# Performance work log

Measured on AMD Instinct MI355X. Metric: run time of the kernel, lower is better.

Reference implementation:

```python
import jax, jax.numpy as jnp
import numpy as np

SHIFT, REDUCE = 1, 2
B, L, E, H = 128, 64, 512, 512
T = 2 * L - 1  # valid binary-parse transition sequence length


def _make_transitions(rng):
    # Random *valid* shift-reduce sequences: L shifts, L-1 reduces, stack ends at 1.
    trans = np.zeros((B, T), dtype=np.int32)
    for b in range(B):
        stack, buf = 0, L
        for t in range(T):
            ops_left = T - t
            can_shift = buf > 0 and stack < ops_left
            can_reduce = stack >= 2
            if can_shift and can_reduce:
                act = SHIFT if rng.random() < 0.5 else REDUCE
            elif can_shift:
                act = SHIFT
            else:
                act = REDUCE
            if act == SHIFT:
                buf -= 1; stack += 1
            else:
                stack -= 1
            trans[b, t] = act
    return trans


def setup_inputs() -> dict:
    key = jax.random.key(0)
    k1, k2, k3, k4 = jax.random.split(key, 4)
    sentence = jax.random.normal(k1, (B, L, E), dtype=jnp.float32)
    transitions = jnp.asarray(_make_transitions(np.random.default_rng(0)))
    W_word = jax.random.normal(k2, (E, 2 * H), dtype=jnp.float32) / np.sqrt(E).astype(np.float32)
    b_word = jnp.zeros((2 * H,), dtype=jnp.float32)
    W_left = jax.random.normal(k3, (H, 5 * H), dtype=jnp.float32) / np.sqrt(H).astype(np.float32)
    W_right = jax.random.normal(k4, (H, 5 * H), dtype=jnp.float32) / np.sqrt(H).astype(np.float32)
    b_reduce = jnp.zeros((5 * H,), dtype=jnp.float32)
    return {"sentence": sentence, "transitions": transitions, "W_word": W_word,
            "b_word": b_word, "W_left": W_left, "W_right": W_right, "b_reduce": b_reduce}


def reference(sentence, transitions, W_word, b_word, W_left, W_right, b_reduce):
    Bx, Lx, _ = sentence.shape
    Hx = W_left.shape[0]
    Tx = transitions.shape[1]
    # word projection (no_batch_norm=True, dropout=0 in this config)
    out = sentence @ W_word + b_word                      # [B, L, 2H]
    h_buf, c_buf = jnp.split(out, 2, axis=2)              # buffers, popped front-to-back
    rows = jnp.arange(Bx)
    ops_left_seq = jnp.arange(Tx, 0, -1, dtype=jnp.int32)
    init = (jnp.zeros((Bx, Lx, Hx), out.dtype),           # stack h
            jnp.zeros((Bx, Lx, Hx), out.dtype),           # stack c
            jnp.zeros((Bx,), jnp.int32),                  # stack ptr
            jnp.zeros((Bx,), jnp.int32))                  # buffer ptr

    def step(carry, xs):
        sh, sc, sp, bp = carry
        act, ops = xs
        act = jnp.where(sp > ops, REDUCE, act)            # forced reduce (discrete stack)
        is_red = act == REDUCE
        is_shf = act == SHIFT
        r_idx = jnp.clip(sp - 1, 0, Lx - 1)
        l_idx = jnp.clip(sp - 2, 0, Lx - 1)
        hl, cl = sh[rows, l_idx], sc[rows, l_idx]
        hr, cr = sh[rows, r_idx], sc[rows, r_idx]
        # TreeLSTM Reduce cell
        gates = hl @ W_left + hr @ W_right + b_reduce     # [B, 5H]
        g, i, f1, f2, o = jnp.split(gates, 5, axis=1)
        c_red = jnp.tanh(g) * jax.nn.sigmoid(i) + jax.nn.sigmoid(f1) * cl + jax.nn.sigmoid(f2) * cr
        h_red = jax.nn.sigmoid(o) * jnp.tanh(c_red)
        b_idx = jnp.clip(bp, 0, Lx - 1)
        h_shf, c_shf = h_buf[rows, b_idx], c_buf[rows, b_idx]
        w_idx = jnp.where(is_red, l_idx, jnp.clip(sp, 0, Lx - 1))
        h_cur, c_cur = sh[rows, w_idx], sc[rows, w_idx]
        m_red, m_shf = is_red[:, None], is_shf[:, None]
        wh = jnp.where(m_red, h_red, jnp.where(m_shf, h_shf, h_cur))
        wc = jnp.where(m_red, c_red, jnp.where(m_shf, c_shf, c_cur))
        sh = sh.at[rows, w_idx].set(wh)
        sc = sc.at[rows, w_idx].set(wc)
        sp = sp + is_shf.astype(jnp.int32) - is_red.astype(jnp.int32)
        bp = bp + is_shf.astype(jnp.int32)
        return (sh, sc, sp, bp), None

    (sh, sc, sp, bp), _ = jax.lax.scan(step, init, (transitions.T, ops_left_seq))
    return sh[rows, jnp.clip(sp - 1, 0, Lx - 1)]          # [B, H] top of each stack
```

## Files before the change

### kernel.cpp

```cpp
#include <hip/hip_runtime.h>
#include <hip/hip_bf16.h>


#define Bn 128
#define Ln 64
#define En 512
#define Hn 512
#define Tn 127
#define LEAF_ROWS (Bn*Ln)
#define NODE_ROWS (Bn*(Ln-1))
#define TOT_ROWS (LEAF_ROWS+NODE_ROWS)
#define NLVL 64
#define NXCD 8
#define CAPX 512
#define NBLK 512
#define FPAD 16
#define MAXRANK 96
#define SPIN_CAP (1<<22)
#define GATE_STRIDE (512*1024)
#define WLDS_BYTES 65536
#define PART_BYTES (4*2*16*20*4)
#define DYN_BYTES (WLDS_BYTES + PART_BYTES)

#define OFF_CENSUS 0
#define OFF_RANK   (OFF_CENSUS + NXCD*FPAD)
#define OFF_SFLAG  (OFF_RANK + NBLK*FPAD)
#define OFF_SGEN   (OFF_SFLAG + NBLK*FPAD)
#define OFF_FX     (OFF_SGEN + FPAD)
#define OFF_GX     (OFF_FX + NXCD*MAXRANK*FPAD)
#define BAR_INTS   (OFF_GX + NXCD*FPAD)

typedef __attribute__((ext_vector_type(8))) short bf16x8;
typedef __attribute__((ext_vector_type(4))) float f32x4;

static __device__ __forceinline__ float bf2f(unsigned short u){
  unsigned v = ((unsigned)u) << 16;
  float f; __builtin_memcpy(&f, &v, 4); return f;
}
static __device__ __forceinline__ unsigned short f2bf(float f){
  unsigned u; __builtin_memcpy(&u, &f, 4);
  u = u + 0x7FFFu + ((u >> 16) & 1u);
  return (unsigned short)(u >> 16);
}
static __device__ __forceinline__ float sigm(float x){
  return 1.0f / (1.0f + __expf(-x));
}
static __device__ __forceinline__ float tanh_fast(float x){
  x = fminf(fmaxf(x, -15.0f), 15.0f);
  float t = __expf(2.0f * x);
  return (t - 1.0f) / (t + 1.0f);
}
static __device__ __forceinline__ int xcc_id(){
  unsigned v;
  asm volatile("s_getreg_b32 %0, hwreg(HW_REG_XCC_ID)" : "=s"(v));
  return (int)(v & 7);
}

static __device__ __forceinline__ void xcd_barrier(int* bar, int x, int rank, int nx, int epoch){
  __syncthreads();
  int* fx = bar + OFF_FX + x * MAXRANK * FPAD;
  int* gx = bar + OFF_GX + x * FPAD;
  int nxl = min(nx, MAXRANK);
  if (rank == 0){
    for (int i = threadIdx.x + 1; i < nxl; i += 256){
      int c = 0;
      while (__hip_atomic_load(&fx[i * FPAD], __ATOMIC_RELAXED, __HIP_MEMORY_SCOPE_AGENT) < epoch && c < SPIN_CAP){
        __builtin_amdgcn_s_sleep(1); ++c;
      }
    }
    __syncthreads();
    if (threadIdx.x == 0)
      __hip_atomic_store(gx, epoch, __ATOMIC_RELAXED, __HIP_MEMORY_SCOPE_AGENT);
  } else {
    if (threadIdx.x == 0){
      __hip_atomic_store(&fx[rank * FPAD], epoch, __ATOMIC_RELAXED, __HIP_MEMORY_SCOPE_AGENT);
      int c = 0;
      while (__hip_atomic_load(gx, __ATOMIC_RELAXED, __HIP_MEMORY_SCOPE_AGENT) < epoch && c < SPIN_CAP){
        __builtin_amdgcn_s_sleep(2); ++c;
      }
    }
    __syncthreads();
  }
  asm volatile("" ::: "memory");
}


__global__ void cvt_vec4(const float4* __restrict__ x, ushort4* __restrict__ y, int n4){
  int i = blockIdx.x * 256 + threadIdx.x;
  if (i < n4){
    float4 v = x[i];
    ushort4 o;
    o.x = f2bf(v.x); o.y = f2bf(v.y); o.z = f2bf(v.z); o.w = f2bf(v.w);
    y[i] = o;
  }
}

__global__ void transpose_cvt(const float* __restrict__ src, unsigned short* __restrict__ dstT,
                              int CS, int DS, int koff){
  __shared__ float tile[32][33];
  int c0 = blockIdx.x * 32, r0 = blockIdx.y * 32;
  int tx = threadIdx.x, ty = threadIdx.y;
  for (int i = ty; i < 32; i += 8) tile[i][tx] = src[(size_t)(r0 + i) * CS + c0 + tx];
  __syncthreads();
  for (int i = ty; i < 32; i += 8)
    dstT[(size_t)(c0 + i) * DS + koff + r0 + tx] = f2bf(tile[tx][i]);
}

__global__ void precompute_ctrl(const int* __restrict__ trans,
                                int* __restrict__ srcL, int* __restrict__ srcR,
                                int* __restrict__ dstv, int* __restrict__ cnt,
                                int* __restrict__ outsrc, int* __restrict__ bar){
  __shared__ int stk[Bn][Ln + 1];
  __shared__ int scnt[NXCD * NLVL];
  __shared__ int smaxl[NXCD];
  int b = threadIdx.x;
  for (int i = b; i < NXCD * NLVL; i += 128) scnt[i] = 0;
  if (b < NXCD) smaxl[b] = 0;
  for (int i = b; i < BAR_INTS; i += 128) bar[i] = 0;
  __syncthreads();
  int x = b & 7;
  int sp = 0, bp = 0, nodecnt = 0;
  int act_next = trans[b * Tn];
  for (int t = 0; t < Tn; t++){
    int act = act_next;
    if (t + 1 < Tn) act_next = trans[b * Tn + t + 1];
    int ops = Tn - t;
    if (sp > ops) act = 2;
    if (act == 2){
      int R = stk[b][sp - 1], L = stk[b][sp - 2];
      int lvl = max(R >> 20, L >> 20) + 1;
      int slot = atomicAdd(&scnt[x * NLVL + lvl], 1);
      int base = (x * NLVL + lvl) * CAPX + slot;
      srcL[base] = (L & 0xFFFFF) * Hn;
      srcR[base] = (R & 0xFFFFF) * Hn;
      int noderow = LEAF_ROWS + b * (Ln - 1) + nodecnt;
      dstv[base] = noderow * Hn;
      stk[b][sp - 2] = noderow | (lvl << 20);
      sp -= 1; nodecnt++;
    } else {
      stk[b][sp] = b * Ln + min(bp, Ln - 1);
      sp += 1; bp += 1;
    }
  }
  int root = stk[b][max(sp - 1, 0)];
  outsrc[b] = (root & 0xFFFFF) * Hn;
  atomicMax(&smaxl[x], root >> 20);
  __syncthreads();
  for (int i = b; i < NXCD * NLVL; i += 128) cnt[i] = scnt[i];
  if (b < NXCD) cnt[NXCD * NLVL + b] = smaxl[b];
}

__global__ __launch_bounds__(256) void word_gemm(
    const unsigned short* __restrict__ SB, const unsigned short* __restrict__ WwT,
    const float* __restrict__ b_word,
    unsigned short* __restrict__ HB, float* __restrict__ CF){
  int mt = blockIdx.x;
  int nt = blockIdx.y;
  int tid = threadIdx.x, w = tid >> 6, lane = tid & 63;
  int wm = w >> 1, wn = w & 1;
  int rc = lane & 15, lg = lane >> 4;
  const unsigned short* ap0 = SB + (size_t)(mt * 64 + wm * 32 + rc) * En + lg * 8;
  const unsigned short* ap1 = ap0 + (size_t)16 * En;
  const unsigned short* bp0 = WwT + (size_t)(nt * 128 + wn * 64 + rc) * En + lg * 8;
  f32x4 acc[2][4];
  #pragma unroll
  for (int h = 0; h < 2; h++)
    #pragma unroll
    for (int nb = 0; nb < 4; nb++) acc[h][nb] = (f32x4){0.f,0.f,0.f,0.f};

  bf16x8 a0c = *(const bf16x8*)ap0;
  bf16x8 a1c = *(const bf16x8*)ap1;
  bf16x8 bc[4];
  #pragma unroll
  for (int nb = 0; nb < 4; nb++) bc[nb] = *(const bf16x8*)(bp0 + (size_t)nb * 16 * En);

  #pragma unroll
  for (int j = 0; j < 16; ++j){
    bf16x8 a0n, a1n, bn[4];
    if (j < 15){
      int kn = (j + 1) * 32;
      a0n = *(const bf16x8*)(ap0 + kn);
      a1n = *(const bf16x8*)(ap1 + kn);
      #pragma unroll
      for (int nb = 0; nb < 4; nb++)
        bn[nb] = *(const bf16x8*)(bp0 + (size_t)nb * 16 * En + kn);
    }
    #pragma unroll
    for (int nb = 0; nb < 4; nb++){
      acc[0][nb] = __builtin_amdgcn_mfma_f32_16x16x32_bf16(a0c, bc[nb], acc[0][nb], 0, 0, 0);
      acc[1][nb] = __builtin_amdgcn_mfma_f32_16x16x32_bf16(a1c, bc[nb], acc[1][nb], 0, 0, 0);
    }
    a0c = a0n; a1c = a1n;
    #pragma unroll
    for (int nb = 0; nb < 4; nb++) bc[nb] = bn[nb];
  }
  #pragma unroll
  for (int nb = 0; nb < 4; nb++){
    int col = nt * 128 + wn * 64 + nb * 16 + rc;
    float bw = b_word[col];
    #pragma unroll
    for (int h = 0; h < 2; h++){
      #pragma unroll
      for (int q = 0; q < 4; q++){
        int row = mt * 64 + wm * 32 + h * 16 + lg * 4 + q;
        float v = acc[h][nb][q] + bw;
        if (col < Hn) HB[(size_t)row * Hn + col] = f2bf(v);
        else          CF[(size_t)row * Hn + (col - Hn)] = v;
      }
    }
  }
}

template<bool LDSB>
static __device__ __forceinline__ void tile64(
    int u0, int t, int nr, const int* __restrict__ sL, const int* __restrict__ sR,
    const int* __restrict__ dl,
    unsigned short* __restrict__ HB, float* __restrict__ CF,
    const unsigned short* __restrict__ WT, const float* __restrict__ b_red,
    const unsigned short* __restrict__ wlds, int rc, int lg)
{
  int base = t * 64;
  int offL[4], offR[4];
  #pragma unroll
  for (int m = 0; m < 4; m++){
    int i = min(base + m * 16 + rc, nr - 1);
    offL[m] = sL[i]; offR[m] = sR[i];
  }
  f32x4 acc[5][4];
  #pragma unroll
  for (int g = 0; g < 5; g++)
    #pragma unroll
    for (int m = 0; m < 4; m++) acc[g][m] = (f32x4){0.f,0.f,0.f,0.f};

  int bswz = (rc & 7) << 3;
  const unsigned short* gb = WT + (size_t)(u0 + rc) * 1024 + lg * 8;

  bf16x8 a_cur[4], b_cur[3];
  #pragma unroll
  for (int m = 0; m < 4; m++) a_cur[m] = *(const bf16x8*)(HB + offL[m] + lg * 8);
  #pragma unroll
  for (int g = 0; g < 3; g++)
    b_cur[g] = *(const bf16x8*)(gb + (size_t)(g + 2) * GATE_STRIDE);

  #pragma unroll 4
  for (int j = 0; j < 32; ++j){
    bf16x8 a_nxt[4], b_nxt[3];
    if (j < 31){
      int kn = (j + 1) * 32 + lg * 8;
      #pragma unroll
      for (int m = 0; m < 4; m++){
        const unsigned short* ap = (j + 1 < 16) ? (HB + offL[m] + kn) : (HB + offR[m] + (kn - 512));
        a_nxt[m] = *(const bf16x8*)ap;
      }
      #pragma unroll
      for (int g = 0; g < 3; g++)
        b_nxt[g] = *(const bf16x8*)(gb + (size_t)(g + 2) * GATE_STRIDE + (j + 1) * 32);
    }
    int k = j * 32 + lg * 8;
    #pragma unroll
    for (int g = 0; g < 2; g++){
      bf16x8 bb;
      if (LDSB) bb = *(const bf16x8*)&wlds[(size_t)(g * 16 + rc) * 1024 + (k ^ bswz)];
      else      bb = *(const bf16x8*)(gb + (size_t)g * GATE_STRIDE + j * 32);
      #pragma unroll
      for (int m = 0; m < 4; m++)
        acc[g][m] = __builtin_amdgcn_mfma_f32_16x16x32_bf16(a_cur[m], bb, acc[g][m], 0, 0, 0);
    }
    #pragma unroll
    for (int g = 0; g < 3; g++){
      #pragma unroll
      for (int m = 0; m < 4; m++)
        acc[g + 2][m] = __builtin_amdgcn_mfma_f32_16x16x32_bf16(a_cur[m], b_cur[g], acc[g + 2][m], 0, 0, 0);
    }
    #pragma unroll
    for (int m = 0; m < 4; m++) a_cur[m] = a_nxt[m];
    #pragma unroll
    for (int g = 0; g < 3; g++) b_cur[g] = b_nxt[g];
  }
  int colu = u0 + rc;
  float bs[5];
  #pragma unroll
  for (int g = 0; g < 5; g++) bs[g] = b_red[g * Hn + colu];
  #pragma unroll
  for (int m = 0; m < 4; m++){
    #pragma unroll
    for (int q = 0; q < 4; q++){
      int i = base + m * 16 + lg * 4 + q;
      if (i < nr){
        int oL = sL[i], oR = sR[i], oD = dl[i];
        float gv = tanh_fast(acc[0][m][q] + bs[0]);
        float iv = sigm(acc[1][m][q] + bs[1]);
        float f1 = sigm(acc[2][m][q] + bs[2]);
        float f2 = sigm(acc[3][m][q] + bs[3]);
        float ov = sigm(acc[4][m][q] + bs[4]);
        float cl = __builtin_nontemporal_load(CF + oL + colu);
        float cr = __builtin_nontemporal_load(CF + oR + colu);
        float cv = gv * iv + f1 * cl + f2 * cr;
        float hv = ov * tanh_fast(cv);
        __builtin_nontemporal_store(cv, CF + oD + colu);
        HB[oD + colu] = f2bf(hv);
      }
    }
  }
}

static __device__ __forceinline__ void tile16(
    int u0, int t, int nr, const int* __restrict__ sL, const int* __restrict__ sR,
    const int* __restrict__ dl,
    unsigned short* __restrict__ HB, float* __restrict__ CF,
    const unsigned short* __restrict__ WT, const float* __restrict__ b_red,
    const unsigned short* __restrict__ wlds, float (*part)[2][16][20],
    int tid, int w, int rc, int lg)
{
  int base = t * 16;
  int er = tid >> 4, eu = tid & 15;
  int i0 = min(base + rc, nr - 1);
  int offA = (w >= 2) ? sR[i0] : sL[i0];
  int ie = min(base + er, nr - 1);
  int oL = sL[ie], oR = sR[ie], oD = dl[ie];
  int colu = u0 + eu;
  float cl = __builtin_nontemporal_load(CF + oL + colu);
  float cr = __builtin_nontemporal_load(CF + oR + colu);

  int k0 = w * 256;
  int abase = (w >= 2) ? (k0 - 512) : k0;
  const unsigned short* ap = HB + offA + abase + lg * 8;
  int bswz = (rc & 7) << 3;
  const unsigned short* gb = WT + (size_t)(u0 + rc) * 1024;

  f32x4 acc[5];
  #pragma unroll
  for (int g = 0; g < 5; g++) acc[g] = (f32x4){0.f,0.f,0.f,0.f};

  bf16x8 a_cur = *(const bf16x8*)ap;
  bf16x8 b_cur[3];
  #pragma unroll
  for (int g = 0; g < 3; g++)
    b_cur[g] = *(const bf16x8*)(gb + (size_t)(g + 2) * GATE_STRIDE + k0 + lg * 8);

  #pragma unroll
  for (int j = 0; j < 8; ++j){
    bf16x8 a_nxt, b_nxt[3];
    if (j < 7){
      a_nxt = *(const bf16x8*)(ap + (j + 1) * 32);
      #pragma unroll
      for (int g = 0; g < 3; g++)
        b_nxt[g] = *(const bf16x8*)(gb + (size_t)(g + 2) * GATE_STRIDE + k0 + (j + 1) * 32 + lg * 8);
    }
    int k = k0 + j * 32 + lg * 8;
    #pragma unroll
    for (int g = 0; g < 2; g++){
      bf16x8 bb = *(const bf16x8*)&wlds[(size_t)(g * 16 + rc) * 1024 + (k ^ bswz)];
      acc[g] = __builtin_amdgcn_mfma_f32_16x16x32_bf16(a_cur, bb, acc[g], 0, 0, 0);
    }
    #pragma unroll
    for (int g = 0; g < 3; g++)
      acc[g + 2] = __builtin_amdgcn_mfma_f32_16x16x32_bf16(a_cur, b_cur[g], acc[g + 2], 0, 0, 0);
    a_cur = a_nxt;
    #pragma unroll
    for (int g = 0; g < 3; g++) b_cur[g] = b_nxt[g];
  }
  float sg[5];
  #pragma unroll
  for (int r = 0; r < 3; ++r){
    int ng = (r < 2) ? 2 : 1;
    #pragma unroll
    for (int gi = 0; gi < 2; ++gi){
      if (gi < ng){
        int g = r * 2 + gi;
        #pragma unroll
        for (int q = 0; q < 4; q++) part[w][gi][lg * 4 + q][rc] = acc[g][q];
      }
    }
    __syncthreads();
    #pragma unroll
    for (int gi = 0; gi < 2; ++gi){
      if (gi < ng)
        sg[r * 2 + gi] = part[0][gi][er][eu] + part[1][gi][er][eu]
                       + part[2][gi][er][eu] + part[3][gi][er][eu];
    }
    __syncthreads();
  }
  int i = base + er;
  if (i < nr){
    float gv = tanh_fast(sg[0] + b_red[colu]);
    float iv = sigm(sg[1] + b_red[Hn + colu]);
    float f1 = sigm(sg[2] + b_red[2 * Hn + colu]);
    float f2 = sigm(sg[3] + b_red[3 * Hn + colu]);
    float ov = sigm(sg[4] + b_red[4 * Hn + colu]);
    float cv = gv * iv + f1 * cl + f2 * cr;
    float hv = ov * tanh_fast(cv);
    __builtin_nontemporal_store(cv, CF + oD + colu);
    HB[oD + colu] = f2bf(hv);
  }
  __syncthreads();
}

extern __shared__ char dynbuf[];

__global__ __launch_bounds__(256, 2) void tree_kernel(
    unsigned short* __restrict__ HB, float* __restrict__ CF,
    const unsigned short* __restrict__ WT, const float* __restrict__ b_red,
    const int* __restrict__ srcL, const int* __restrict__ srcR,
    const int* __restrict__ dstv, const int* __restrict__ cnt,
    const int* __restrict__ outsrc, float* __restrict__ out, int* bar){
  unsigned short* wlds = (unsigned short*)dynbuf;
  float (*part)[2][16][20] = (float(*)[2][16][20])(dynbuf + WLDS_BYTES);
  int bid = blockIdx.x;
  int tid = threadIdx.x, w = tid >> 6, lane = tid & 63;
  int rc = lane & 15, lg = lane >> 4;

  int x = xcc_id();
  if (tid == 0){
    int r = __hip_atomic_fetch_add(&bar[OFF_CENSUS + x * FPAD], 1,
                                   __ATOMIC_RELAXED, __HIP_MEMORY_SCOPE_AGENT);
    __hip_atomic_store(&bar[OFF_RANK + bid * FPAD], r, __ATOMIC_RELAXED, __HIP_MEMORY_SCOPE_AGENT);
  }
  __syncthreads();
  int rank = min(__hip_atomic_load(&bar[OFF_RANK + bid * FPAD], __ATOMIC_RELAXED, __HIP_MEMORY_SCOPE_AGENT),
                 MAXRANK - 1);
  int ub = rank & 31;
  int u0 = ub * 16;

  for (int gg = tid; gg < 4096; gg += 256){
    int row = gg >> 7;
    int k = (gg & 127) * 8;
    int u = row & 15, g = row >> 4;
    bf16x8 v = *(const bf16x8*)(WT + (size_t)(g * 512 + u0 + u) * 1024 + k);
    int kx = k ^ ((u & 7) << 3);
    *(bf16x8*)&wlds[(size_t)row * 1024 + kx] = v;
  }
  __syncthreads();

  {
    int* sfl  = bar + OFF_SFLAG;
    int* sgen = bar + OFF_SGEN;
    if (bid == 0){
      for (int i = tid; i < NBLK; i += 256){
        if (i){
          int c = 0;
          while (__hip_atomic_load(&sfl[i * FPAD], __ATOMIC_RELAXED, __HIP_MEMORY_SCOPE_AGENT) == 0 && c < SPIN_CAP){
            __builtin_amdgcn_s_sleep(1); ++c;
          }
        }
      }
      __syncthreads();
      if (tid == 0) __hip_atomic_store(sgen, 1, __ATOMIC_RELAXED, __HIP_MEMORY_SCOPE_AGENT);
    } else {
      if (tid == 0){
        __hip_atomic_store(&sfl[bid * FPAD], 1, __ATOMIC_RELAXED, __HIP_MEMORY_SCOPE_AGENT);
        int c = 0;
        while (__hip_atomic_load(sgen, __ATOMIC_RELAXED, __HIP_MEMORY_SCOPE_AGENT) == 0 && c < SPIN_CAP){
          __builtin_amdgcn_s_sleep(2); ++c;
        }
      }
      __syncthreads();
    }
  }
  int nx = max(__hip_atomic_load(&bar[OFF_CENSUS + x * FPAD], __ATOMIC_RELAXED, __HIP_MEMORY_SCOPE_AGENT), 1);

  int maxlvl = cnt[NXCD * NLVL + x];
  int epoch = 1;
  for (int lvl = 1; lvl <= maxlvl; ++lvl, ++epoch){
    int nr = cnt[x * NLVL + lvl];
    const int* sL = srcL + (x * NLVL + lvl) * CAPX;
    const int* sR = srcR + (x * NLVL + lvl) * CAPX;
    const int* dl = dstv + (x * NLVL + lvl) * CAPX;
    if (nr > 0){
      if (nx >= 32){
        int nstr = (nx - 1 - ub) / 32 + 1;
        int stripe = rank >> 5;
        if (nr >= 128){
          int ntl = (nr + 63) >> 6;
          for (int t = stripe * 4 + w; t < ntl; t += nstr * 4)
            tile64<true>(u0, t, nr, sL, sR, dl, HB, CF, WT, b_red, wlds, rc, lg);
        } else {
          int ntl16 = (nr + 15) >> 4;
          for (int t = stripe; t < ntl16; t += nstr)
            tile16(u0, t, nr, sL, sR, dl, HB, CF, WT, b_red, wlds, part, tid, w, rc, lg);
        }
      } else {
        int ntl = (nr + 63) >> 6;
        int nwv = nx * 4, wid = rank * 4 + w;
        int ntask = ntl * 32;
        for (int task = wid; task < ntask; task += nwv)
          tile64<false>((task / ntl) * 16, task % ntl, nr, sL, sR, dl, HB, CF, WT, b_red, wlds, rc, lg);
      }
    }
    xcd_barrier(bar, x, rank, nx, epoch);
  }

  for (int j = rank; j < 16; j += min(nx, MAXRANK)){
    int b = x + 8 * j;
    int src = outsrc[b];
    out[b * Hn + tid]       = bf2f(HB[src + tid]);
    out[b * Hn + tid + 256] = bf2f(HB[src + tid + 256]);
  }
}

extern "C" void kernel_launch(void* const* d_in, const int* in_sizes, int n_in,
                              void* d_out, int out_size, void* d_ws, size_t ws_size,
                              hipStream_t stream){
  (void)in_sizes; (void)n_in; (void)out_size; (void)ws_size;
  const float* sentence = (const float*)d_in[0];
  const int*   trans    = (const int*)d_in[1];
  const float* W_word   = (const float*)d_in[2];
  const float* b_word   = (const float*)d_in[3];
  const float* W_left   = (const float*)d_in[4];
  const float* W_right  = (const float*)d_in[5];
  const float* b_red    = (const float*)d_in[6];

  char* ws = (char*)d_ws;
  size_t off = 0;
  auto alloc = [&](size_t bytes) -> void* {
    void* p = ws + off;
    off += (bytes + 255) & ~((size_t)255);
    return p;
  };
  unsigned short* HB  = (unsigned short*)alloc((size_t)TOT_ROWS * Hn * 2);
  float*          CF  = (float*)alloc((size_t)TOT_ROWS * Hn * 4);
  unsigned short* WT  = (unsigned short*)alloc((size_t)2560 * 1024 * 2);
  unsigned short* SB  = (unsigned short*)alloc((size_t)LEAF_ROWS * En * 2);
  unsigned short* WwT = (unsigned short*)alloc((size_t)1024 * En * 2);
  int* srcL   = (int*)alloc((size_t)NXCD * NLVL * CAPX * 4);
  int* srcR   = (int*)alloc((size_t)NXCD * NLVL * CAPX * 4);
  int* dstv   = (int*)alloc((size_t)NXCD * NLVL * CAPX * 4);
  int* cnt    = (int*)alloc((size_t)(NXCD * NLVL + NXCD) * 4);
  int* outsrc = (int*)alloc((size_t)Bn * 4);
  int* bar    = (int*)alloc((size_t)BAR_INTS * 4);
  float* outp = (float*)d_out;

  hipFuncSetAttribute(reinterpret_cast<const void*>(tree_kernel),
                      hipFuncAttributeMaxDynamicSharedMemorySize, DYN_BYTES);

  cvt_vec4<<<(LEAF_ROWS * En / 4) / 256, 256, 0, stream>>>((const float4*)sentence, (ushort4*)SB, LEAF_ROWS * En / 4);
  transpose_cvt<<<dim3(1024 / 32, En / 32), dim3(32, 8), 0, stream>>>(W_word, WwT, 1024, En, 0);
  transpose_cvt<<<dim3(2560 / 32, Hn / 32), dim3(32, 8), 0, stream>>>(W_left, WT, 2560, 1024, 0);
  transpose_cvt<<<dim3(2560 / 32, Hn / 32), dim3(32, 8), 0, stream>>>(W_right, WT, 2560, 1024, 512);
  precompute_ctrl<<<1, 128, 0, stream>>>(trans, srcL, srcR, dstv, cnt, outsrc, bar);
  word_gemm<<<dim3(128, 8), 256, 0, stream>>>(SB, WwT, b_word, HB, CF);
  tree_kernel<<<NBLK, 256, DYN_BYTES, stream>>>(HB, CF, WT, b_red, srcL, srcR, dstv, cnt, outsrc, outp, bar);
}
```

Measured before the change: 609.0 us.

## Replace per-level XCD barriers with per-node readiness flags in tree tail

Precompute, per XCD, the level where node counts drop below 128 and, for nodes beyond it, the child node indices. In those tail levels, blocks skip the XCD-wide barrier and instead spin on per-node completion counters, which reach 32 once all column stripes are written. Producers increment the counter after storing their tile, and the final output read waits on the root's counter. This targets the barrier latency across many sparsely populated late levels. In exchange it adds spin-wait overhead and relies on relaxed atomics for memory ordering, with no explicit fences.

```diff
diff --git a/kernel.cpp b/kernel.cpp
--- a/kernel.cpp
+++ b/kernel.cpp
@@ -17,6 +17,7 @@
 #define FPAD 16
 #define MAXRANK 96
 #define SPIN_CAP (1<<22)
+#define WSPIN (1<<20)
 #define GATE_STRIDE (512*1024)
 #define WLDS_BYTES 65536
 #define PART_BYTES (4*2*16*20*4)
@@ -108,15 +109,19 @@
 
 __global__ void precompute_ctrl(const int* __restrict__ trans,
                                 int* __restrict__ srcL, int* __restrict__ srcR,
+                                int* __restrict__ srcLW, int* __restrict__ srcRW,
                                 int* __restrict__ dstv, int* __restrict__ cnt,
-                                int* __restrict__ outsrc, int* __restrict__ bar){
+                                int* __restrict__ outsrc, int* __restrict__ rootW,
+                                int* __restrict__ nf, int* __restrict__ bar){
   __shared__ int stk[Bn][Ln + 1];
   __shared__ int scnt[NXCD * NLVL];
   __shared__ int smaxl[NXCD];
+  __shared__ int stail[NXCD];
   int b = threadIdx.x;
   for (int i = b; i < NXCD * NLVL; i += 128) scnt[i] = 0;
   if (b < NXCD) smaxl[b] = 0;
   for (int i = b; i < BAR_INTS; i += 128) bar[i] = 0;
+  for (int i = b; i < NODE_ROWS; i += 128) nf[i] = 0;
   __syncthreads();
   int x = b & 7;
   int sp = 0, bp = 0, nodecnt = 0;
@@ -133,6 +138,8 @@
       int base = (x * NLVL + lvl) * CAPX + slot;
       srcL[base] = (L & 0xFFFFF) * Hn;
       srcR[base] = (R & 0xFFFFF) * Hn;
+      srcLW[base] = L >> 20;
+      srcRW[base] = R >> 20;
       int noderow = LEAF_ROWS + b * (Ln - 1) + nodecnt;
       dstv[base] = noderow * Hn;
       stk[b][sp - 2] = noderow | (lvl << 20);
@@ -146,8 +153,32 @@
   outsrc[b] = (root & 0xFFFFF) * Hn;
   atomicMax(&smaxl[x], root >> 20);
   __syncthreads();
+  if (b < NXCD){
+    int ts = NLVL;
+    for (int l = 1; l < NLVL; l++){
+      if (scnt[b * NLVL + l] < 128){ ts = l; break; }
+    }
+    stail[b] = max(ts, 2);
+  }
+  __syncthreads();
+  for (int p = b; p < NXCD * NLVL; p += 128){
+    int px = p / NLVL, lvl = p - px * NLVL;
+    int n = scnt[p], ts = stail[px];
+    for (int s = 0; s < n; s++){
+      int idx = p * CAPX + s;
+      int ll = srcLW[idx], rl = srcRW[idx];
+      srcLW[idx] = (lvl >= ts && ll >= ts) ? ((srcL[idx] >> 9) - LEAF_ROWS) : -1;
+      srcRW[idx] = (lvl >= ts && rl >= ts) ? ((srcR[idx] >> 9) - LEAF_ROWS) : -1;
+    }
+  }
+  int rlvl = root >> 20;
+  rootW[b] = (rlvl >= stail[x]) ? ((root & 0xFFFFF) - LEAF_ROWS) : -1;
+  __syncthreads();
   for (int i = b; i < NXCD * NLVL; i += 128) cnt[i] = scnt[i];
-  if (b < NXCD) cnt[NXCD * NLVL + b] = smaxl[b];
+  if (b < NXCD){
+    cnt[NXCD * NLVL + b] = smaxl[b];
+    cnt[NXCD * NLVL + NXCD + b] = stail[b];
+  }
 }
 
 __global__ __launch_bounds__(256) void word_gemm(
@@ -304,9 +335,11 @@
   }
 }
 
+template<bool FLAGS>
 static __device__ __forceinline__ void tile16(
     int u0, int t, int nr, const int* __restrict__ sL, const int* __restrict__ sR,
     const int* __restrict__ dl,
+    const int* __restrict__ sLW, const int* __restrict__ sRW, int* __restrict__ nf,
     unsigned short* __restrict__ HB, float* __restrict__ CF,
     const unsigned short* __restrict__ WT, const float* __restrict__ b_red,
     const unsigned short* __restrict__ wlds, float (*part)[2][16][20],
@@ -314,6 +347,22 @@
 {
   int base = t * 16;
   int er = tid >> 4, eu = tid & 15;
+  if (FLAGS){
+    int rr = min(base + (tid & 15), nr - 1);
+    int wl = sLW[rr], wr = sRW[rr];
+    int c = 0;
+    if (wl >= 0){
+      while (__hip_atomic_load(&nf[wl], __ATOMIC_RELAXED, __HIP_MEMORY_SCOPE_AGENT) < 32 && c < WSPIN){
+        __builtin_amdgcn_s_sleep(1); ++c;
+      }
+    }
+    c = 0;
+    if (wr >= 0){
+      while (__hip_atomic_load(&nf[wr], __ATOMIC_RELAXED, __HIP_MEMORY_SCOPE_AGENT) < 32 && c < WSPIN){
+        __builtin_amdgcn_s_sleep(1); ++c;
+      }
+    }
+  }
   int i0 = min(base + rc, nr - 1);
   int offA = (w >= 2) ? sR[i0] : sL[i0];
   int ie = min(base + er, nr - 1);
@@ -394,6 +443,11 @@
     HB[oD + colu] = f2bf(hv);
   }
   __syncthreads();
+  if (FLAGS){
+    if (tid < 16 && base + tid < nr)
+      __hip_atomic_fetch_add(&nf[(dl[base + tid] >> 9) - LEAF_ROWS], 1,
+                             __ATOMIC_RELAXED, __HIP_MEMORY_SCOPE_AGENT);
+  }
 }
 
 extern __shared__ char dynbuf[];
@@ -402,8 +456,10 @@
     unsigned short* __restrict__ HB, float* __restrict__ CF,
     const unsigned short* __restrict__ WT, const float* __restrict__ b_red,
     const int* __restrict__ srcL, const int* __restrict__ srcR,
+    const int* __restrict__ srcLW, const int* __restrict__ srcRW,
     const int* __restrict__ dstv, const int* __restrict__ cnt,
-    const int* __restrict__ outsrc, float* __restrict__ out, int* bar){
+    const int* __restrict__ outsrc, const int* __restrict__ rootW,
+    int* __restrict__ nf, float* __restrict__ out, int* bar){
   unsigned short* wlds = (unsigned short*)dynbuf;
   float (*part)[2][16][20] = (float(*)[2][16][20])(dynbuf + WLDS_BYTES);
   int bid = blockIdx.x;
@@ -459,15 +515,26 @@
   }
   int nx = max(__hip_atomic_load(&bar[OFF_CENSUS + x * FPAD], __ATOMIC_RELAXED, __HIP_MEMORY_SCOPE_AGENT), 1);
 
-  int maxlvl = cnt[NXCD * NLVL + x];
+  int maxlvl   = cnt[NXCD * NLVL + x];
+  int tailStart = cnt[NXCD * NLVL + NXCD + x];
+  bool flagmode = (nx >= 32);
   int epoch = 1;
-  for (int lvl = 1; lvl <= maxlvl; ++lvl, ++epoch){
+  for (int lvl = 1; lvl <= maxlvl; ++lvl){
     int nr = cnt[x * NLVL + lvl];
-    const int* sL = srcL + (x * NLVL + lvl) * CAPX;
-    const int* sR = srcR + (x * NLVL + lvl) * CAPX;
-    const int* dl = dstv + (x * NLVL + lvl) * CAPX;
+    const int* sL  = srcL  + (x * NLVL + lvl) * CAPX;
+    const int* sR  = srcR  + (x * NLVL + lvl) * CAPX;
+    const int* sLW = srcLW + (x * NLVL + lvl) * CAPX;
+    const int* sRW = srcRW + (x * NLVL + lvl) * CAPX;
+    const int* dl  = dstv  + (x * NLVL + lvl) * CAPX;
+    bool tailmode = flagmode && (lvl >= tailStart);
     if (nr > 0){
-      if (nx >= 32){
+      if (tailmode){
+        int nstr = (nx - 1 - ub) / 32 + 1;
+        int stripe = rank >> 5;
+        int ntl16 = (nr + 15) >> 4;
+        for (int t = stripe; t < ntl16; t += nstr)
+          tile16<true>(u0, t, nr, sL, sR, dl, sLW, sRW, nf, HB, CF, WT, b_red, wlds, part, tid, w, rc, lg);
+      } else if (flagmode){
         int nstr = (nx - 1 - ub) / 32 + 1;
         int stripe = rank >> 5;
         if (nr >= 128){
@@ -477,7 +544,7 @@
         } else {
           int ntl16 = (nr + 15) >> 4;
           for (int t = stripe; t < ntl16; t += nstr)
-            tile16(u0, t, nr, sL, sR, dl, HB, CF, WT, b_red, wlds, part, tid, w, rc, lg);
+            tile16<false>(u0, t, nr, sL, sR, dl, sLW, sRW, nf, HB, CF, WT, b_red, wlds, part, tid, w, rc, lg);
         }
       } else {
         int ntl = (nr + 63) >> 6;
@@ -487,11 +554,23 @@
           tile64<false>((task / ntl) * 16, task % ntl, nr, sL, sR, dl, HB, CF, WT, b_red, wlds, rc, lg);
       }
     }
-    xcd_barrier(bar, x, rank, nx, epoch);
+    if (!tailmode){
+      xcd_barrier(bar, x, rank, nx, epoch);
+      ++epoch;
+    }
   }
 
   for (int j = rank; j < 16; j += min(nx, MAXRANK)){
     int b = x + 8 * j;
+    if (flagmode){
+      int rw = rootW[b];
+      if (rw >= 0){
+        int c = 0;
+        while (__hip_atomic_load(&nf[rw], __ATOMIC_RELAXED, __HIP_MEMORY_SCOPE_AGENT) < 32 && c < WSPIN){
+          __builtin_amdgcn_s_sleep(1); ++c;
+        }
+      }
+    }
     int src = outsrc[b];
     out[b * Hn + tid]       = bf2f(HB[src + tid]);
     out[b * Hn + tid + 256] = bf2f(HB[src + tid + 256]);
@@ -524,9 +603,13 @@
   unsigned short* WwT = (unsigned short*)alloc((size_t)1024 * En * 2);
   int* srcL   = (int*)alloc((size_t)NXCD * NLVL * CAPX * 4);
   int* srcR   = (int*)alloc((size_t)NXCD * NLVL * CAPX * 4);
+  int* srcLW  = (int*)alloc((size_t)NXCD * NLVL * CAPX * 4);
+  int* srcRW  = (int*)alloc((size_t)NXCD * NLVL * CAPX * 4);
   int* dstv   = (int*)alloc((size_t)NXCD * NLVL * CAPX * 4);
-  int* cnt    = (int*)alloc((size_t)(NXCD * NLVL + NXCD) * 4);
+  int* cnt    = (int*)alloc((size_t)(NXCD * NLVL + 2 * NXCD) * 4);
   int* outsrc = (int*)alloc((size_t)Bn * 4);
+  int* rootW  = (int*)alloc((size_t)Bn * 4);
+  int* nf     = (int*)alloc((size_t)NODE_ROWS * 4);
   int* bar    = (int*)alloc((size_t)BAR_INTS * 4);
   float* outp = (float*)d_out;
 
@@ -537,7 +620,8 @@
   transpose_cvt<<<dim3(1024 / 32, En / 32), dim3(32, 8), 0, stream>>>(W_word, WwT, 1024, En, 0);
   transpose_cvt<<<dim3(2560 / 32, Hn / 32), dim3(32, 8), 0, stream>>>(W_left, WT, 2560, 1024, 0);
   transpose_cvt<<<dim3(2560 / 32, Hn / 32), dim3(32, 8), 0, stream>>>(W_right, WT, 2560, 1024, 512);
-  precompute_ctrl<<<1, 128, 0, stream>>>(trans, srcL, srcR, dstv, cnt, outsrc, bar);
+  precompute_ctrl<<<1, 128, 0, stream>>>(trans, srcL, srcR, srcLW, srcRW, dstv, cnt, outsrc, rootW, nf, bar);
   word_gemm<<<dim3(128, 8), 256, 0, stream>>>(SB, WwT, b_word, HB, CF);
-  tree_kernel<<<NBLK, 256, DYN_BYTES, stream>>>(HB, CF, WT, b_red, srcL, srcR, dstv, cnt, outsrc, outp, bar);
-}
+  tree_kernel<<<NBLK, 256, DYN_BYTES, stream>>>(HB, CF, WT, b_red, srcL, srcR, srcLW, srcRW,
+                                                dstv, cnt, outsrc, rootW, nf, outp, bar);
+}
```

Result: slower. 864.1 us (+41.9%).
